# Optimization experiments

Measured on AMD Instinct MI355X. Metric: run time of the kernel, lower is better.

## Reference

```python
import jax, jax.numpy as jnp
import numpy as np

N_NODES = 20000
N_EDGES = 200000
MUL = 16          # multiplicity of 0e and 1o in irreps_in/out
NUM_BASIS = 8
HIDDEN = 64
W_NUMEL = 4 * MUL * MUL  # 1024: four 'uvw' paths of 16x1x16 weights
INV_SQRT3 = 1.0 / np.sqrt(3.0)
PW0 = np.sqrt(1.0 / 32.0)  # path weight into 0e: sqrt(dim(0e)/(16+16))
PW1 = np.sqrt(3.0 / 32.0)  # path weight into 1o: sqrt(dim(1o)/(16+16))
SI_NORM = 1.0 / np.sqrt(MUL)  # o3.Linear fan-in normalization


def setup_inputs() -> dict:
    key = jax.random.key(0)
    ks = jax.random.split(key, 12)
    node_feat = jax.random.normal(ks[0], (N_NODES, 4 * MUL), dtype=jnp.float32)
    edge_attr = jax.random.uniform(ks[1], (N_EDGES, NUM_BASIS), dtype=jnp.float32)
    sh = jax.random.normal(ks[2], (N_EDGES, 4), dtype=jnp.float32)
    edge_index = jax.random.randint(ks[3], (2, N_EDGES), 0, N_NODES, dtype=jnp.int32)
    # radial MLP params (torch nn.Linear: y = x @ W.T + b; we store W already transposed)
    w1 = jax.random.normal(ks[4], (NUM_BASIS, HIDDEN), dtype=jnp.float32) * 0.3
    b1 = jax.random.normal(ks[5], (HIDDEN,), dtype=jnp.float32) * 0.1
    w2 = jax.random.normal(ks[6], (HIDDEN, W_NUMEL), dtype=jnp.float32) * 0.1
    b2 = jax.random.normal(ks[7], (W_NUMEL,), dtype=jnp.float32) * 0.1
    # o3.Linear self-interaction: one (mul_in, mul_out) block per irrep
    wsi0 = jax.random.normal(ks[8], (MUL, MUL), dtype=jnp.float32)
    wsi1 = jax.random.normal(ks[9], (MUL, MUL), dtype=jnp.float32)
    return {"node_feat": node_feat, "edge_attr": edge_attr, "sh": sh,
            "w1": w1, "b1": b1, "w2": w2, "b2": b2,
            "wsi0": wsi0, "wsi1": wsi1, "edge_index": edge_index}


def reference(node_feat, edge_attr, sh, w1, b1, w2, b2, wsi0, wsi1, edge_index):
    n_nodes = node_feat.shape[0]
    row, col = edge_index[0], edge_index[1]

    # per-edge tensor-product weights from radial basis
    h = jax.nn.silu(edge_attr @ w1 + b1)
    w = h @ w2 + b2                                   # [E, 1024]
    Wp = w.reshape(-1, 4, MUL, MUL)                    # 4 paths, each (u, w)

    # gathered source-node features, split into 0e scalars and 1o vectors
    xs = node_feat[col, :MUL]                          # [E, 16]
    xv = node_feat[col, MUL:].reshape(-1, MUL, 3)      # [E, 16, 3]
    y0 = sh[:, 0]                                      # [E]   0e part of sh
    y1 = sh[:, 1:4]                                    # [E,3] 1o part of sh

    # CG paths (e3nn FullyConnectedTensorProduct, component/element norm):
    # path0: 0e x 0e -> 0e (cg=1); path3: 1o x 1o -> 0e (cg=delta/sqrt3)
    dot = jnp.einsum('eum,em->eu', xv, y1)             # [E,16]
    out0 = PW0 * (jnp.einsum('euw,eu->ew', Wp[:, 0], xs * y0[:, None])
                  + INV_SQRT3 * jnp.einsum('euw,eu->ew', Wp[:, 3], dot))
    # path1: 0e x 1o -> 1o; path2: 1o x 0e -> 1o (cg=delta/sqrt3)
    outv = (PW1 * INV_SQRT3) * (
        jnp.einsum('euw,eu->ew', Wp[:, 1], xs)[:, :, None] * y1[:, None, :]
        + jnp.einsum('euw,eum->ewm', Wp[:, 2], xv) * y0[:, None, None])

    messages = jnp.concatenate([out0, outv.reshape(-1, 3 * MUL)], axis=-1)  # [E,64]
    agg = jax.ops.segment_sum(messages, row, num_segments=n_nodes)          # [N,64]

    # self-interaction: o3.Linear (block-diagonal per irrep, / sqrt(fan_in))
    si0 = (node_feat[:, :MUL] @ wsi0) * SI_NORM
    siv = jnp.einsum('num,uw->nwm', node_feat[:, MUL:].reshape(-1, MUL, 3), wsi1) * SI_NORM
    si = jnp.concatenate([si0, siv.reshape(-1, 3 * MUL)], axis=-1)
    return agg + si
```

## Files before the change

kernel.cpp:

```cpp
#include <hip/hip_runtime.h>
#include <hip/hip_bf16.h>

#define N_NODES_C 20000
#define N_EDGES_C 200000

#define PW0_C       0.17677669529663687f
#define PW1_C       0.30618621784789724f
#define INV_SQRT3_C 0.57735026918962576f
#define SI_NORM_C   0.25f

typedef __attribute__((ext_vector_type(8))) short short8;
typedef __attribute__((ext_vector_type(4))) float f32x4;

__device__ __forceinline__ unsigned short f2bf(float x) {
    union { float f; unsigned u; } v; v.f = x;
    unsigned r = v.u + 0x7fffu + ((v.u >> 16) & 1u);
    return (unsigned short)(r >> 16);
}
__device__ __forceinline__ float bf2f(unsigned short v) {
    union { unsigned u; float f; } x; x.u = ((unsigned)v) << 16; return x.f;
}

__global__ __launch_bounds__(256) void k_h(const float* __restrict__ ea,
                                           const float* __restrict__ w1,
                                           const float* __restrict__ b1,
                                           unsigned short* __restrict__ h) {
    int idx = blockIdx.x * 256 + threadIdx.x;
    int e = idx >> 6, c = idx & 63;
    const float* a = ea + e * 8;
    float acc = b1[c];
    #pragma unroll
    for (int k = 0; k < 8; ++k) acc = fmaf(a[k], w1[k * 64 + c], acc);
    float s = acc / (1.0f + __expf(-acc));
    h[idx] = f2bf(s);
}

__global__ __launch_bounds__(256) void k_w2(const float* __restrict__ w2,
                                            unsigned short* __restrict__ w2f) {
    int tid = blockIdx.x * 256 + threadIdx.x;
    int j  = tid & 7;
    int l  = (tid >> 3) & 63;
    int ks = (tid >> 9) & 1;
    int tp = tid >> 10;
    int u = tp >> 2, k = tp & 3;
    int krow = ks * 32 + (l >> 4) * 8 + j;
    int col  = k * 256 + u * 16 + (l & 15);
    w2f[tid] = f2bf(w2[krow * 1024 + col]);
}

__global__ __launch_bounds__(256) void k_count(const int* __restrict__ ei,
                                               int* __restrict__ cnt) {
    int e = blockIdx.x * 256 + threadIdx.x;
    if (e < N_EDGES_C) atomicAdd(&cnt[ei[e]], 1);
}

__global__ __launch_bounds__(1024) void k_scan(const int* __restrict__ cnt,
                                               int* __restrict__ base) {
    __shared__ int wsum[16];
    __shared__ int carry_s;
    if (threadIdx.x == 0) carry_s = 0;
    int lane = threadIdx.x & 63, wid = threadIdx.x >> 6;
    __syncthreads();
    for (int start = 0; start < N_NODES_C; start += 1024) {
        int i = start + threadIdx.x;
        int v = (i < N_NODES_C) ? cnt[i] : 0;
        int x = v;
        #pragma unroll
        for (int d = 1; d < 64; d <<= 1) {
            int y = __shfl_up(x, d);
            if (lane >= d) x += y;
        }
        if (lane == 63) wsum[wid] = x;
        __syncthreads();
        int woff = 0;
        #pragma unroll
        for (int w = 0; w < 16; ++w) if (w < wid) woff += wsum[w];
        int carry = carry_s;
        if (i < N_NODES_C) base[i] = carry + woff + x - v;
        __syncthreads();
        if (threadIdx.x == 1023) carry_s = carry + woff + x;
    }
    if (threadIdx.x == 0) base[N_NODES_C] = N_EDGES_C;
}

__global__ __launch_bounds__(256) void k_fill(const int* __restrict__ ei,
                                              const int* __restrict__ base,
                                              int* __restrict__ cur,
                                              int* __restrict__ eix) {
    int e = blockIdx.x * 256 + threadIdx.x;
    if (e < N_EDGES_C) {
        int r = ei[e];
        int p = atomicAdd(&cur[r], 1);
        eix[base[r] + p] = e;
    }
}

__global__ void __launch_bounds__(256) __attribute__((amdgpu_waves_per_eu(2, 2)))
k_main(const float* __restrict__ nf,
       const float* __restrict__ sh,
       const int* __restrict__ ei,
       const int* __restrict__ eix,
       const unsigned short* __restrict__ h,
       const unsigned short* __restrict__ w2f,
       const float* __restrict__ b2,
       unsigned short* __restrict__ msgb) {
    __shared__ __align__(16) char EXraw[24576];
    __shared__ float S[6][16][64];
    __shared__ float sh_s[64][4];
    __shared__ float b2_s[4][16][16];

    float (*nf_s)[64]  = (float (*)[64])EXraw;
    float (*P0)[16]    = (float (*)[16])EXraw;
    float (*P1)[16]    = (float (*)[16])(EXraw + 4096);
    float (*P3)[16]    = (float (*)[16])(EXraw + 8192);
    float (*Q)[64][16] = (float (*)[64][16])(EXraw + 12288);

    const int t    = threadIdx.x;
    const int e0   = blockIdx.x * 64;
    const int lane = t & 63;
    const int wid  = t >> 6;

    {
        float* b2flat = &b2_s[0][0][0];
        #pragma unroll
        for (int i = 0; i < 4; ++i) b2flat[t + i * 256] = b2[t + i * 256];
        int el = t >> 2, part = t & 3;
        int ep  = eix[e0 + el];
        int col = ei[N_EDGES_C + ep];
        const f32x4* src = (const f32x4*)(nf + (size_t)col * 64);
        #pragma unroll
        for (int q = 0; q < 4; ++q)
            *(f32x4*)&nf_s[el][part * 16 + q * 4] = src[part * 4 + q];
        if (part == 0)
            *(f32x4*)&sh_s[el][0] = *(const f32x4*)(sh + (size_t)ep * 4);
    }
    short8 B0[16], B1[16];
    {
        const unsigned short* wk = w2f + wid * 1024 + lane * 8;
        #pragma unroll
        for (int u = 0; u < 16; ++u) {
            B0[u] = *(const short8*)&wk[u * 4096];
            B1[u] = *(const short8*)&wk[u * 4096 + 512];
        }
    }
    __syncthreads();

    {
        int el = t >> 2, part = t & 3;
        float y0 = sh_s[el][0], y1x = sh_s[el][1], y1y = sh_s[el][2], y1z = sh_s[el][3];
        #pragma unroll
        for (int uu = 0; uu < 4; ++uu) {
            int u = part * 4 + uu;
            float xs = nf_s[el][u];
            float v0 = nf_s[el][16 + u * 3 + 0];
            float v1 = nf_s[el][16 + u * 3 + 1];
            float v2 = nf_s[el][16 + u * 3 + 2];
            float dot = v0 * y1x + v1 * y1y + v2 * y1z;
            S[0][u][el] = xs * y0;
            S[1][u][el] = xs;
            S[2][u][el] = v0;
            S[3][u][el] = v1;
            S[4][u][el] = v2;
            S[5][u][el] = INV_SQRT3_C * dot;
        }
    }
    __syncthreads();

    const int wcol = lane & 15;
    const int g4   = (lane >> 4) << 2;

    #define TILE_PROLOG(tt)                                                        \
        int epl = eix[e0 + (tt) * 16 + (lane & 15)];                               \
        const unsigned short* hrow = h + (size_t)epl * 64 + ((lane >> 4) * 8);     \
        short8 a0 = *(const short8*)(hrow);                                        \
        short8 a1 = *(const short8*)(hrow + 32);

    if (wid == 0) {
        #pragma unroll 1
        for (int tt = 0; tt < 4; ++tt) {
            TILE_PROLOG(tt)
            f32x4 acc = {0.f, 0.f, 0.f, 0.f};
            #pragma unroll
            for (int u = 0; u < 16; ++u) {
                f32x4 c = {0.f, 0.f, 0.f, 0.f};
                c = __builtin_amdgcn_mfma_f32_16x16x32_bf16(a0, B0[u], c, 0, 0, 0);
                c = __builtin_amdgcn_mfma_f32_16x16x32_bf16(a1, B1[u], c, 0, 0, 0);
                float bb = b2_s[0][u][wcol];
                f32x4 s = *(const f32x4*)&S[0][u][tt * 16 + g4];
                #pragma unroll
                for (int r = 0; r < 4; ++r) acc[r] = fmaf(c[r] + bb, s[r], acc[r]);
            }
            #pragma unroll
            for (int r = 0; r < 4; ++r) P0[tt * 16 + g4 + r][wcol] = acc[r];
        }
    } else if (wid == 1) {
        #pragma unroll 1
        for (int tt = 0; tt < 4; ++tt) {
            TILE_PROLOG(tt)
            f32x4 acc = {0.f, 0.f, 0.f, 0.f};
            #pragma unroll
            for (int u = 0; u < 16; ++u) {
                f32x4 c = {0.f, 0.f, 0.f, 0.f};
                c = __builtin_amdgcn_mfma_f32_16x16x32_bf16(a0, B0[u], c, 0, 0, 0);
                c = __builtin_amdgcn_mfma_f32_16x16x32_bf16(a1, B1[u], c, 0, 0, 0);
                float bb = b2_s[1][u][wcol];
                f32x4 s = *(const f32x4*)&S[1][u][tt * 16 + g4];
                #pragma unroll
                for (int r = 0; r < 4; ++r) acc[r] = fmaf(c[r] + bb, s[r], acc[r]);
            }
            #pragma unroll
            for (int r = 0; r < 4; ++r) P1[tt * 16 + g4 + r][wcol] = acc[r];
        }
    } else if (wid == 2) {
        #pragma unroll 1
        for (int tt = 0; tt < 4; ++tt) {
            TILE_PROLOG(tt)
            f32x4 qa = {0.f,0.f,0.f,0.f}, qb = {0.f,0.f,0.f,0.f}, qc = {0.f,0.f,0.f,0.f};
            #pragma unroll
            for (int u = 0; u < 16; ++u) {
                f32x4 c = {0.f, 0.f, 0.f, 0.f};
                c = __builtin_amdgcn_mfma_f32_16x16x32_bf16(a0, B0[u], c, 0, 0, 0);
                c = __builtin_amdgcn_mfma_f32_16x16x32_bf16(a1, B1[u], c, 0, 0, 0);
                float bb = b2_s[2][u][wcol];
                f32x4 s0 = *(const f32x4*)&S[2][u][tt * 16 + g4];
                f32x4 s1 = *(const f32x4*)&S[3][u][tt * 16 + g4];
                f32x4 s2 = *(const f32x4*)&S[4][u][tt * 16 + g4];
                #pragma unroll
                for (int r = 0; r < 4; ++r) {
                    float wp = c[r] + bb;
                    qa[r] = fmaf(wp, s0[r], qa[r]);
                    qb[r] = fmaf(wp, s1[r], qb[r]);
                    qc[r] = fmaf(wp, s2[r], qc[r]);
                }
            }
            #pragma unroll
            for (int r = 0; r < 4; ++r) {
                Q[0][tt * 16 + g4 + r][wcol] = qa[r];
                Q[1][tt * 16 + g4 + r][wcol] = qb[r];
                Q[2][tt * 16 + g4 + r][wcol] = qc[r];
            }
        }
    } else {
        #pragma unroll 1
        for (int tt = 0; tt < 4; ++tt) {
            TILE_PROLOG(tt)
            f32x4 acc = {0.f, 0.f, 0.f, 0.f};
            #pragma unroll
            for (int u = 0; u < 16; ++u) {
                f32x4 c = {0.f, 0.f, 0.f, 0.f};
                c = __builtin_amdgcn_mfma_f32_16x16x32_bf16(a0, B0[u], c, 0, 0, 0);
                c = __builtin_amdgcn_mfma_f32_16x16x32_bf16(a1, B1[u], c, 0, 0, 0);
                float bb = b2_s[3][u][wcol];
                f32x4 s = *(const f32x4*)&S[5][u][tt * 16 + g4];
                #pragma unroll
                for (int r = 0; r < 4; ++r) acc[r] = fmaf(c[r] + bb, s[r], acc[r]);
            }
            #pragma unroll
            for (int r = 0; r < 4; ++r) P3[tt * 16 + g4 + r][wcol] = acc[r];
        }
    }
    #undef TILE_PROLOG
    __syncthreads();

    {
        int c  = t & 63;
        int eg = t >> 6;
        if (c < 16) {
            #pragma unroll
            for (int i = 0; i < 16; ++i) {
                int e = eg * 16 + i;
                msgb[(size_t)(e0 + e) * 64 + c] = f2bf(PW0_C * (P0[e][c] + P3[e][c]));
            }
        } else {
            const float c1 = PW1_C * INV_SQRT3_C;
            int w = (c - 16) / 3, m = (c - 16) - 3 * w;
            #pragma unroll
            for (int i = 0; i < 16; ++i) {
                int e = eg * 16 + i;
                msgb[(size_t)(e0 + e) * 64 + c] =
                    f2bf(c1 * (P1[e][w] * sh_s[e][1 + m] + Q[m][e][w] * sh_s[e][0]));
            }
        }
    }
}

__global__ __launch_bounds__(256) void k_gather(const unsigned short* __restrict__ msgb,
                                                const int* __restrict__ base,
                                                const float* __restrict__ nf,
                                                const float* __restrict__ wsi0,
                                                const float* __restrict__ wsi1,
                                                float* __restrict__ out) {
    int wid = threadIdx.x >> 6, lane = threadIdx.x & 63;
    int n = blockIdx.x * 4 + wid;
    if (n >= N_NODES_C) return;
    int j0 = base[n], j1 = base[n + 1];
    int d = j1 - j0;
    const unsigned short* p = msgb + (size_t)j0 * 64 + lane;
    float acc = 0.f;
    int j = 0;
    for (; j + 4 <= d; j += 4) {
        unsigned short v0 = p[(size_t)(j + 0) * 64];
        unsigned short v1 = p[(size_t)(j + 1) * 64];
        unsigned short v2 = p[(size_t)(j + 2) * 64];
        unsigned short v3 = p[(size_t)(j + 3) * 64];
        acc += (bf2f(v0) + bf2f(v1)) + (bf2f(v2) + bf2f(v3));
    }
    for (; j < d; ++j) acc += bf2f(p[(size_t)j * 64]);
    const float* x = nf + (size_t)n * 64;
    float si = 0.f;
    if (lane < 16) {
        #pragma unroll
        for (int u = 0; u < 16; ++u) si = fmaf(x[u], wsi0[u * 16 + lane], si);
    } else {
        int w = (lane - 16) / 3, m = (lane - 16) - w * 3;
        #pragma unroll
        for (int u = 0; u < 16; ++u) si = fmaf(x[16 + u * 3 + m], wsi1[u * 16 + w], si);
    }
    out[(size_t)n * 64 + lane] = acc + si * SI_NORM_C;
}

extern "C" void kernel_launch(void* const* d_in, const int* in_sizes, int n_in,
                              void* d_out, int out_size, void* d_ws, size_t ws_size,
                              hipStream_t stream) {
    const float* nf   = (const float*)d_in[0];
    const float* ea   = (const float*)d_in[1];
    const float* sh   = (const float*)d_in[2];
    const float* w1   = (const float*)d_in[3];
    const float* b1   = (const float*)d_in[4];
    const float* w2   = (const float*)d_in[5];
    const float* b2   = (const float*)d_in[6];
    const float* wsi0 = (const float*)d_in[7];
    const float* wsi1 = (const float*)d_in[8];
    const int*   ei   = (const int*)d_in[9];
    float* out = (float*)d_out;

    char* ws = (char*)d_ws;
    unsigned short* msgb = (unsigned short*)ws;
    unsigned short* h    = (unsigned short*)(ws + 25600000);
    unsigned short* w2f  = (unsigned short*)(ws + 51200000);
    int* cnt             = (int*)(ws + 51331072);
    int* cur             = cnt + N_NODES_C;
    int* base            = cur + N_NODES_C;
    int* eix             = base + N_NODES_C + 1;

    hipMemsetAsync(cnt, 0, 2 * N_NODES_C * sizeof(int), stream);

    k_h    <<<50000, 256, 0, stream>>>(ea, w1, b1, h);
    k_w2   <<<256,   256, 0, stream>>>(w2, w2f);
    k_count<<<(N_EDGES_C + 255) / 256, 256, 0, stream>>>(ei, cnt);
    k_scan <<<1,    1024, 0, stream>>>(cnt, base);
    k_fill <<<(N_EDGES_C + 255) / 256, 256, 0, stream>>>(ei, base, cur, eix);
    k_main <<<3125,  256, 0, stream>>>(nf, sh, ei, eix, h, w2f, b2, msgb);
    k_gather<<<5000, 256, 0, stream>>>(msgb, base, nf, wsi0, wsi1, out);
}
```

Measured before the change: 206.5 us.

## Fuse radial MLP hidden layer into main kernel and split u-range across 8 waves

The separate k_h kernel, which wrote a bf16 hidden activation buffer to global memory, is removed; each k_main block now loads edge_attr and computes the SiLU hidden layer into shared memory. The block grows to 512 threads, with two wave halves each covering 8 of the 16 u indices and combining partial results through shared-memory atomics. The per-edge scalars in shared memory are stored as bf16 to save space, and the gather loop is unrolled to 8. This removes a global write and read of the hidden tensor and one launch, at the cost of LDS atomics, an extra zeroing pass and some precision loss in the scalars.

```diff
diff --git a/kernel.cpp b/kernel.cpp
--- a/kernel.cpp
+++ b/kernel.cpp
@@ -19,20 +19,6 @@
 }
 __device__ __forceinline__ float bf2f(unsigned short v) {
     union { unsigned u; float f; } x; x.u = ((unsigned)v) << 16; return x.f;
-}
-
-__global__ __launch_bounds__(256) void k_h(const float* __restrict__ ea,
-                                           const float* __restrict__ w1,
-                                           const float* __restrict__ b1,
-                                           unsigned short* __restrict__ h) {
-    int idx = blockIdx.x * 256 + threadIdx.x;
-    int e = idx >> 6, c = idx & 63;
-    const float* a = ea + e * 8;
-    float acc = b1[c];
-    #pragma unroll
-    for (int k = 0; k < 8; ++k) acc = fmaf(a[k], w1[k * 64 + c], acc);
-    float s = acc / (1.0f + __expf(-acc));
-    h[idx] = f2bf(s);
 }
 
 __global__ __launch_bounds__(256) void k_w2(const float* __restrict__ w2,
@@ -95,73 +81,106 @@
     }
 }
 
-__global__ void __launch_bounds__(256) __attribute__((amdgpu_waves_per_eu(2, 2)))
+#define HS_PAD 80
+__global__ __launch_bounds__(512) void
 k_main(const float* __restrict__ nf,
+       const float* __restrict__ ea,
        const float* __restrict__ sh,
        const int* __restrict__ ei,
        const int* __restrict__ eix,
-       const unsigned short* __restrict__ h,
+       const float* __restrict__ w1,
+       const float* __restrict__ b1,
        const unsigned short* __restrict__ w2f,
        const float* __restrict__ b2,
        unsigned short* __restrict__ msgb) {
-    __shared__ __align__(16) char EXraw[24576];
-    __shared__ float S[6][16][64];
+    __shared__ __align__(16) char R1[26112];
+    __shared__ __align__(16) unsigned short S_bf[6][16][64];
+    __shared__ __align__(16) unsigned short hs[64][HS_PAD];
     __shared__ float sh_s[64][4];
     __shared__ float b2_s[4][16][16];
 
-    float (*nf_s)[64]  = (float (*)[64])EXraw;
-    float (*P0)[16]    = (float (*)[16])EXraw;
-    float (*P1)[16]    = (float (*)[16])(EXraw + 4096);
-    float (*P3)[16]    = (float (*)[16])(EXraw + 8192);
-    float (*Q)[64][16] = (float (*)[64][16])(EXraw + 12288);
+    float (*nf_s)[64] = (float (*)[64])R1;
+    float (*ea_s)[8]  = (float (*)[8])(R1 + 16384);
+    float (*P)[64][17] = (float (*)[64][17])R1;
 
     const int t    = threadIdx.x;
-    const int e0   = blockIdx.x * 64;
     const int lane = t & 63;
     const int wid  = t >> 6;
+    const int kcls = wid & 3;
+    const int half = wid >> 2;
+    const int e0   = blockIdx.x * 64;
+
+    const int el   = t >> 3;
+    const int part = t & 7;
 
     {
         float* b2flat = &b2_s[0][0][0];
-        #pragma unroll
-        for (int i = 0; i < 4; ++i) b2flat[t + i * 256] = b2[t + i * 256];
-        int el = t >> 2, part = t & 3;
+        b2flat[t] = b2[t];
+        b2flat[t + 512] = b2[t + 512];
         int ep  = eix[e0 + el];
         int col = ei[N_EDGES_C + ep];
         const f32x4* src = (const f32x4*)(nf + (size_t)col * 64);
-        #pragma unroll
-        for (int q = 0; q < 4; ++q)
-            *(f32x4*)&nf_s[el][part * 16 + q * 4] = src[part * 4 + q];
+        *(f32x4*)&nf_s[el][part * 8]     = src[part * 2];
+        *(f32x4*)&nf_s[el][part * 8 + 4] = src[part * 2 + 1];
+        ea_s[el][part] = ea[(size_t)ep * 8 + part];
         if (part == 0)
             *(f32x4*)&sh_s[el][0] = *(const f32x4*)(sh + (size_t)ep * 4);
     }
-    short8 B0[16], B1[16];
+    short8 B0[8], B1[8];
+    #pragma unroll
+    for (int uu = 0; uu < 8; ++uu) {
+        int u = half * 8 + uu;
+        const unsigned short* wk = w2f + (u * 4 + kcls) * 1024 + lane * 8;
+        B0[uu] = *(const short8*)(wk);
+        B1[uu] = *(const short8*)(wk + 512);
+    }
+    __syncthreads();
+
     {
-        const unsigned short* wk = w2f + wid * 1024 + lane * 8;
-        #pragma unroll
-        for (int u = 0; u < 16; ++u) {
-            B0[u] = *(const short8*)&wk[u * 4096];
-            B1[u] = *(const short8*)&wk[u * 4096 + 512];
-        }
-    }
-    __syncthreads();
-
-    {
-        int el = t >> 2, part = t & 3;
         float y0 = sh_s[el][0], y1x = sh_s[el][1], y1y = sh_s[el][2], y1z = sh_s[el][3];
         #pragma unroll
-        for (int uu = 0; uu < 4; ++uu) {
-            int u = part * 4 + uu;
+        for (int uu = 0; uu < 2; ++uu) {
+            int u = part * 2 + uu;
             float xs = nf_s[el][u];
             float v0 = nf_s[el][16 + u * 3 + 0];
             float v1 = nf_s[el][16 + u * 3 + 1];
             float v2 = nf_s[el][16 + u * 3 + 2];
             float dot = v0 * y1x + v1 * y1y + v2 * y1z;
-            S[0][u][el] = xs * y0;
-            S[1][u][el] = xs;
-            S[2][u][el] = v0;
-            S[3][u][el] = v1;
-            S[4][u][el] = v2;
-            S[5][u][el] = INV_SQRT3_C * dot;
+            S_bf[0][u][el] = f2bf(xs * y0);
+            S_bf[1][u][el] = f2bf(xs);
+            S_bf[2][u][el] = f2bf(v0);
+            S_bf[3][u][el] = f2bf(v1);
+            S_bf[4][u][el] = f2bf(v2);
+            S_bf[5][u][el] = f2bf(INV_SQRT3_C * dot);
+        }
+        float a0 = ea_s[el][0], a1 = ea_s[el][1], a2 = ea_s[el][2], a3 = ea_s[el][3];
+        float a4 = ea_s[el][4], a5 = ea_s[el][5], a6 = ea_s[el][6], a7 = ea_s[el][7];
+        short8 hv;
+        #pragma unroll
+        for (int j = 0; j < 8; ++j) {
+            int c = part * 8 + j;
+            float acc = b1[c];
+            acc = fmaf(a0, w1[0 * 64 + c], acc);
+            acc = fmaf(a1, w1[1 * 64 + c], acc);
+            acc = fmaf(a2, w1[2 * 64 + c], acc);
+            acc = fmaf(a3, w1[3 * 64 + c], acc);
+            acc = fmaf(a4, w1[4 * 64 + c], acc);
+            acc = fmaf(a5, w1[5 * 64 + c], acc);
+            acc = fmaf(a6, w1[6 * 64 + c], acc);
+            acc = fmaf(a7, w1[7 * 64 + c], acc);
+            float s = acc / (1.0f + __expf(-acc));
+            hv[j] = (short)f2bf(s);
+        }
+        *(short8*)&hs[el][part * 8] = hv;
+    }
+    __syncthreads();
+
+    {
+        float* Pf = (float*)R1;
+        #pragma unroll
+        for (int i = 0; i < 13; ++i) {
+            int idx = t + i * 512;
+            if (idx < 6 * 64 * 17) Pf[idx] = 0.f;
         }
     }
     __syncthreads();
@@ -169,97 +188,58 @@
     const int wcol = lane & 15;
     const int g4   = (lane >> 4) << 2;
 
-    #define TILE_PROLOG(tt)                                                        \
-        int epl = eix[e0 + (tt) * 16 + (lane & 15)];                               \
-        const unsigned short* hrow = h + (size_t)epl * 64 + ((lane >> 4) * 8);     \
-        short8 a0 = *(const short8*)(hrow);                                        \
-        short8 a1 = *(const short8*)(hrow + 32);
-
-    if (wid == 0) {
-        #pragma unroll 1
-        for (int tt = 0; tt < 4; ++tt) {
-            TILE_PROLOG(tt)
+    #pragma unroll 1
+    for (int tt = 0; tt < 4; ++tt) {
+        int row = tt * 16 + (lane & 15);
+        short8 a0 = *(const short8*)&hs[row][(lane >> 4) * 8];
+        short8 a1 = *(const short8*)&hs[row][(lane >> 4) * 8 + 32];
+        int eb = tt * 16 + g4;
+        if (kcls != 2) {
+            const int cls = (kcls == 0) ? 0 : (kcls == 1) ? 1 : 5;
             f32x4 acc = {0.f, 0.f, 0.f, 0.f};
             #pragma unroll
-            for (int u = 0; u < 16; ++u) {
+            for (int uu = 0; uu < 8; ++uu) {
+                int u = half * 8 + uu;
                 f32x4 c = {0.f, 0.f, 0.f, 0.f};
-                c = __builtin_amdgcn_mfma_f32_16x16x32_bf16(a0, B0[u], c, 0, 0, 0);
-                c = __builtin_amdgcn_mfma_f32_16x16x32_bf16(a1, B1[u], c, 0, 0, 0);
-                float bb = b2_s[0][u][wcol];
-                f32x4 s = *(const f32x4*)&S[0][u][tt * 16 + g4];
+                c = __builtin_amdgcn_mfma_f32_16x16x32_bf16(a0, B0[uu], c, 0, 0, 0);
+                c = __builtin_amdgcn_mfma_f32_16x16x32_bf16(a1, B1[uu], c, 0, 0, 0);
+                float bb = b2_s[kcls][u][wcol];
+                unsigned long long sv = *(const unsigned long long*)&S_bf[cls][u][eb];
                 #pragma unroll
-                for (int r = 0; r < 4; ++r) acc[r] = fmaf(c[r] + bb, s[r], acc[r]);
-            }
-            #pragma unroll
-            for (int r = 0; r < 4; ++r) P0[tt * 16 + g4 + r][wcol] = acc[r];
-        }
-    } else if (wid == 1) {
-        #pragma unroll 1
-        for (int tt = 0; tt < 4; ++tt) {
-            TILE_PROLOG(tt)
-            f32x4 acc = {0.f, 0.f, 0.f, 0.f};
-            #pragma unroll
-            for (int u = 0; u < 16; ++u) {
+                for (int r = 0; r < 4; ++r)
+                    acc[r] = fmaf(c[r] + bb, bf2f((unsigned short)(sv >> (16 * r))), acc[r]);
+            }
+            #pragma unroll
+            for (int r = 0; r < 4; ++r)
+                atomicAdd(&P[cls][eb + r][wcol], acc[r]);
+        } else {
+            f32x4 qa = {0.f,0.f,0.f,0.f}, qb = {0.f,0.f,0.f,0.f}, qc = {0.f,0.f,0.f,0.f};
+            #pragma unroll
+            for (int uu = 0; uu < 8; ++uu) {
+                int u = half * 8 + uu;
                 f32x4 c = {0.f, 0.f, 0.f, 0.f};
-                c = __builtin_amdgcn_mfma_f32_16x16x32_bf16(a0, B0[u], c, 0, 0, 0);
-                c = __builtin_amdgcn_mfma_f32_16x16x32_bf16(a1, B1[u], c, 0, 0, 0);
-                float bb = b2_s[1][u][wcol];
-                f32x4 s = *(const f32x4*)&S[1][u][tt * 16 + g4];
-                #pragma unroll
-                for (int r = 0; r < 4; ++r) acc[r] = fmaf(c[r] + bb, s[r], acc[r]);
-            }
-            #pragma unroll
-            for (int r = 0; r < 4; ++r) P1[tt * 16 + g4 + r][wcol] = acc[r];
-        }
-    } else if (wid == 2) {
-        #pragma unroll 1
-        for (int tt = 0; tt < 4; ++tt) {
-            TILE_PROLOG(tt)
-            f32x4 qa = {0.f,0.f,0.f,0.f}, qb = {0.f,0.f,0.f,0.f}, qc = {0.f,0.f,0.f,0.f};
-            #pragma unroll
-            for (int u = 0; u < 16; ++u) {
-                f32x4 c = {0.f, 0.f, 0.f, 0.f};
-                c = __builtin_amdgcn_mfma_f32_16x16x32_bf16(a0, B0[u], c, 0, 0, 0);
-                c = __builtin_amdgcn_mfma_f32_16x16x32_bf16(a1, B1[u], c, 0, 0, 0);
+                c = __builtin_amdgcn_mfma_f32_16x16x32_bf16(a0, B0[uu], c, 0, 0, 0);
+                c = __builtin_amdgcn_mfma_f32_16x16x32_bf16(a1, B1[uu], c, 0, 0, 0);
                 float bb = b2_s[2][u][wcol];
-                f32x4 s0 = *(const f32x4*)&S[2][u][tt * 16 + g4];
-                f32x4 s1 = *(const f32x4*)&S[3][u][tt * 16 + g4];
-                f32x4 s2 = *(const f32x4*)&S[4][u][tt * 16 + g4];
+                unsigned long long s0 = *(const unsigned long long*)&S_bf[2][u][eb];
+                unsigned long long s1 = *(const unsigned long long*)&S_bf[3][u][eb];
+                unsigned long long s2 = *(const unsigned long long*)&S_bf[4][u][eb];
                 #pragma unroll
                 for (int r = 0; r < 4; ++r) {
                     float wp = c[r] + bb;
-                    qa[r] = fmaf(wp, s0[r], qa[r]);
-                    qb[r] = fmaf(wp, s1[r], qb[r]);
-                    qc[r] = fmaf(wp, s2[r], qc[r]);
+                    qa[r] = fmaf(wp, bf2f((unsigned short)(s0 >> (16 * r))), qa[r]);
+                    qb[r] = fmaf(wp, bf2f((unsigned short)(s1 >> (16 * r))), qb[r]);
+                    qc[r] = fmaf(wp, bf2f((unsigned short)(s2 >> (16 * r))), qc[r]);
                 }
             }
             #pragma unroll
             for (int r = 0; r < 4; ++r) {
-                Q[0][tt * 16 + g4 + r][wcol] = qa[r];
-                Q[1][tt * 16 + g4 + r][wcol] = qb[r];
-                Q[2][tt * 16 + g4 + r][wcol] = qc[r];
-            }
-        }
-    } else {
-        #pragma unroll 1
-        for (int tt = 0; tt < 4; ++tt) {
-            TILE_PROLOG(tt)
-            f32x4 acc = {0.f, 0.f, 0.f, 0.f};
-            #pragma unroll
-            for (int u = 0; u < 16; ++u) {
-                f32x4 c = {0.f, 0.f, 0.f, 0.f};
-                c = __builtin_amdgcn_mfma_f32_16x16x32_bf16(a0, B0[u], c, 0, 0, 0);
-                c = __builtin_amdgcn_mfma_f32_16x16x32_bf16(a1, B1[u], c, 0, 0, 0);
-                float bb = b2_s[3][u][wcol];
-                f32x4 s = *(const f32x4*)&S[5][u][tt * 16 + g4];
-                #pragma unroll
-                for (int r = 0; r < 4; ++r) acc[r] = fmaf(c[r] + bb, s[r], acc[r]);
-            }
-            #pragma unroll
-            for (int r = 0; r < 4; ++r) P3[tt * 16 + g4 + r][wcol] = acc[r];
-        }
-    }
-    #undef TILE_PROLOG
+                atomicAdd(&P[2][eb + r][wcol], qa[r]);
+                atomicAdd(&P[3][eb + r][wcol], qb[r]);
+                atomicAdd(&P[4][eb + r][wcol], qc[r]);
+            }
+        }
+    }
     __syncthreads();
 
     {
@@ -267,18 +247,18 @@
         int eg = t >> 6;
         if (c < 16) {
             #pragma unroll
-            for (int i = 0; i < 16; ++i) {
-                int e = eg * 16 + i;
-                msgb[(size_t)(e0 + e) * 64 + c] = f2bf(PW0_C * (P0[e][c] + P3[e][c]));
+            for (int i = 0; i < 8; ++i) {
+                int e = eg * 8 + i;
+                msgb[(size_t)(e0 + e) * 64 + c] = f2bf(PW0_C * (P[0][e][c] + P[5][e][c]));
             }
         } else {
             const float c1 = PW1_C * INV_SQRT3_C;
             int w = (c - 16) / 3, m = (c - 16) - 3 * w;
             #pragma unroll
-            for (int i = 0; i < 16; ++i) {
-                int e = eg * 16 + i;
+            for (int i = 0; i < 8; ++i) {
+                int e = eg * 8 + i;
                 msgb[(size_t)(e0 + e) * 64 + c] =
-                    f2bf(c1 * (P1[e][w] * sh_s[e][1 + m] + Q[m][e][w] * sh_s[e][0]));
+                    f2bf(c1 * (P[1][e][w] * sh_s[e][1 + m] + P[2 + m][e][w] * sh_s[e][0]));
             }
         }
     }
@@ -298,12 +278,11 @@
     const unsigned short* p = msgb + (size_t)j0 * 64 + lane;
     float acc = 0.f;
     int j = 0;
-    for (; j + 4 <= d; j += 4) {
-        unsigned short v0 = p[(size_t)(j + 0) * 64];
-        unsigned short v1 = p[(size_t)(j + 1) * 64];
-        unsigned short v2 = p[(size_t)(j + 2) * 64];
-        unsigned short v3 = p[(size_t)(j + 3) * 64];
-        acc += (bf2f(v0) + bf2f(v1)) + (bf2f(v2) + bf2f(v3));
+    for (; j + 8 <= d; j += 8) {
+        float s = 0.f;
+        #pragma unroll
+        for (int q = 0; q < 8; ++q) s += bf2f(p[(size_t)(j + q) * 64]);
+        acc += s;
     }
     for (; j < d; ++j) acc += bf2f(p[(size_t)j * 64]);
     const float* x = nf + (size_t)n * 64;
@@ -336,20 +315,18 @@
 
     char* ws = (char*)d_ws;
     unsigned short* msgb = (unsigned short*)ws;
-    unsigned short* h    = (unsigned short*)(ws + 25600000);
-    unsigned short* w2f  = (unsigned short*)(ws + 51200000);
-    int* cnt             = (int*)(ws + 51331072);
+    unsigned short* w2f  = (unsigned short*)(ws + 25600000);
+    int* cnt             = (int*)(ws + 25731072);
     int* cur             = cnt + N_NODES_C;
     int* base            = cur + N_NODES_C;
     int* eix             = base + N_NODES_C + 1;
 
     hipMemsetAsync(cnt, 0, 2 * N_NODES_C * sizeof(int), stream);
 
-    k_h    <<<50000, 256, 0, stream>>>(ea, w1, b1, h);
     k_w2   <<<256,   256, 0, stream>>>(w2, w2f);
     k_count<<<(N_EDGES_C + 255) / 256, 256, 0, stream>>>(ei, cnt);
     k_scan <<<1,    1024, 0, stream>>>(cnt, base);
     k_fill <<<(N_EDGES_C + 255) / 256, 256, 0, stream>>>(ei, base, cur, eix);
-    k_main <<<3125,  256, 0, stream>>>(nf, sh, ei, eix, h, w2f, b2, msgb);
+    k_main <<<3125,  512, 0, stream>>>(nf, ea, sh, ei, eix, w1, b1, w2f, b2, msgb);
     k_gather<<<5000, 256, 0, stream>>>(msgb, base, nf, wsi0, wsi1, out);
 }
```

Measured after the change: 328.8 us. +59.2%, slower.
